# Performance work log

Hardware: AMD Instinct MI355X
Metric: run time of the kernel (lower is better)

Reference implementation:

```python
import jax, jax.numpy as jnp
import numpy as np

B, T, V, C, D = 32, 512, 25, 64, 128
EPS = 1e-5


def _shift_indices(num_nodes, ch, sign):
    i = np.arange(num_nodes)[:, None]
    j = np.arange(ch)[None, :]
    idx = (i * ch + j + sign * j * ch) % (ch * num_nodes)
    return jnp.asarray(idx.reshape(-1).astype(np.int32))


def setup_inputs() -> dict:
    key = jax.random.key(0)
    ks = jax.random.split(key, 6)
    return {
        "x0": jax.random.normal(ks[0], (B, T, V, C), jnp.float32),
        "feature_mask": jax.random.normal(ks[1], (1, V, C), jnp.float32) * 0.1,
        "W": jax.random.normal(ks[2], (C, D), jnp.float32) * (1.0 / np.sqrt(D)),
        "lin_b": jax.random.normal(ks[3], (1, 1, D), jnp.float32) * 0.02,
        "bn_gamma": jnp.ones((V * D,), jnp.float32),
        "bn_beta": jnp.zeros((V * D,), jnp.float32),
        "down_w": jax.random.normal(ks[4], (D, C), jnp.float32) * (1.0 / np.sqrt(C)),
        "down_b": jax.random.normal(ks[5], (D,), jnp.float32) * 0.02,
        "dbn_gamma": jnp.ones((D,), jnp.float32),
        "dbn_beta": jnp.zeros((D,), jnp.float32),
        "shift_in": _shift_indices(V, C, +1),
        "shift_out": _shift_indices(V, D, -1),
    }


def reference(x0, feature_mask, W, lin_b, bn_gamma, bn_beta,
              down_w, down_b, dbn_gamma, dbn_beta, shift_in, shift_out):
    b, t, v, c = x0.shape
    d = W.shape[1]
    n = b * t
    # shift-in gather over flattened (V*C) feature axis
    x = x0.reshape(n, v * c)[:, shift_in].reshape(n, v, c)
    # learned feature mask
    x = x * (jnp.tanh(feature_mask) + 1.0)
    # small per-node linear
    x = jnp.einsum('nvc,cd->nvd', x, W) + lin_b
    # shift-out gather
    x = x.reshape(n, v * d)[:, shift_out]
    # BatchNorm1d (training-mode batch stats, biased variance)
    mu = x.mean(0)
    var = x.var(0)
    x = (x - mu) * (bn_gamma / jnp.sqrt(var + EPS)) + bn_beta
    x = x.reshape(b, t, v, d).transpose(0, 3, 1, 2)  # (B, D, T, V)
    # residual down path: 1x1 conv == per-position matmul, then BN2d
    res = jnp.einsum('btvc,dc->btvd', x0, down_w) + down_b
    rmu = res.mean((0, 1, 2))
    rvar = res.var((0, 1, 2))
    res = (res - rmu) * (dbn_gamma / jnp.sqrt(rvar + EPS)) + dbn_beta
    res = res.transpose(0, 3, 1, 2)  # (B, D, T, V)
    return jax.nn.relu(x + res)
```

## Files before the change

kernel.cpp:

```cpp
#include <hip/hip_runtime.h>

#define VC 1600
#define EPSF 1e-5f

#define WS_MASKJ  0
#define WS_WPACK  1600
#define WS_DWPACK 5696
#define WS_ABY    9792
#define WS_ABR    16192
#define WS_COLSUM 16448
#define WS_QY     18048
#define WS_ABY2   1721984
#define WS_Y_SH   3456768
#define WS_R_SH   55885568
#define WS_NEED_BYTES 216628736ULL

typedef __attribute__((ext_vector_type(8))) short s16x8;
typedef __attribute__((ext_vector_type(4))) short s16x4;
typedef __attribute__((ext_vector_type(4))) float f32x4;

__device__ __forceinline__ short f2bf(float f) {
  unsigned u = __builtin_bit_cast(unsigned, f);
  u += 0x7fffu + ((u >> 16) & 1u);
  return (short)(u >> 16);
}
__device__ __forceinline__ float bf2f(short s) {
  unsigned u = ((unsigned)(unsigned short)s) << 16;
  return __builtin_bit_cast(float, u);
}

__device__ __forceinline__ void stage_elem(int j, int base, int vstr, float4 xv,
                                           const float* mj, short* s_raw, short* s_xm) {
  int u = j >> 6, c = j & 63;
  s16x4 pk; pk[0]=f2bf(xv.x); pk[1]=f2bf(xv.y); pk[2]=f2bf(xv.z); pk[3]=f2bf(xv.w);
  *(s16x4*)(s_raw + (base + u*vstr)*72 + c) = pk;
  int v0 = (u - c + 75) % 25;
  float xa[4] = {xv.x, xv.y, xv.z, xv.w};
#pragma unroll
  for (int e = 0; e < 4; e++) {
    int ve = v0 - e; if (ve < 0) ve += 25;
    s_xm[(base + ve*vstr)*72 + c + e] = f2bf(xa[e] * mj[e]);
  }
}

__global__ void k_init(const float* __restrict__ fm, const float* __restrict__ W,
                       const float* __restrict__ dw, float* __restrict__ ws) {
  int g = blockIdx.x * 256 + threadIdx.x;
  if (g < VC) {
    int c = g & 63, jv = g >> 6;
    int v = (jv - c + 75) % 25;
    ws[WS_MASKJ + g] = tanhf(fm[v * 64 + c]) + 1.0f;
    ws[WS_COLSUM + g] = 0.0f;
  }
  if (g < 3328) ws[WS_QY + g] = 0.0f;
  if (g >= 4096 && g < 5120) {
    int idx = g - 4096;
    int frag = idx >> 6, lane = idx & 63;
    int nt = frag >> 1, k = frag & 1, q = lane >> 4, l = lane & 15;
    s16x8 pk;
#pragma unroll
    for (int j = 0; j < 8; j++) {
      int c = k * 32 + q * 8 + j;
      pk[j] = f2bf(W[c * 128 + nt * 16 + l]);
    }
    ((s16x8*)(ws + WS_WPACK))[idx] = pk;
  }
  if (g >= 3328 && g < 4096) {
  }
  if (g >= 5120 - 1024 && g < 5120 && false) {}
  if (blockIdx.x >= 16) {
    int idx = (blockIdx.x - 16) * 256 + threadIdx.x;
    if (idx < 1024) {
      int frag = idx >> 6, lane = idx & 63;
      int nt = frag >> 1, k = frag & 1, q = lane >> 4, l = lane & 15;
      s16x8 pk;
#pragma unroll
      for (int j = 0; j < 8; j++) {
        int c = k * 32 + q * 8 + j;
        pk[j] = f2bf(dw[(nt * 16 + l) * 64 + c]);
      }
      ((s16x8*)(ws + WS_DWPACK))[idx] = pk;
    }
  }
}

__launch_bounds__(256, 2)
__global__ void k_stats(const float* __restrict__ x0, float* __restrict__ ws, int do_store) {
  __shared__ short s_raw[8064];
  __shared__ short s_xm[8064];
  int tid = threadIdx.x;
  int wave = tid >> 6, lane = tid & 63, quad = lane >> 4, l15 = lane & 15;
  for (int t = tid; t < 864; t += 256) { s_raw[7200 + t] = 0; s_xm[7200 + t] = 0; }
  const s16x8* wpack = (const s16x8*)(ws + WS_WPACK);
  const s16x8* dwpack = (const s16x8*)(ws + WS_DWPACK);
  short* wsy = (short*)ws + WS_Y_SH;
  short* wsr = (short*)ws + WS_R_SH;

  int nt0 = wave * 2;
  s16x8 bw[2][2], bd[2][2];
#pragma unroll
  for (int a = 0; a < 2; a++) {
    int nt = nt0 + a;
    bw[a][0] = wpack[(nt * 2 + 0) * 64 + lane];
    bw[a][1] = wpack[(nt * 2 + 1) * 64 + lane];
    bd[a][0] = dwpack[(nt * 2 + 0) * 64 + lane];
    bd[a][1] = dwpack[(nt * 2 + 1) * 64 + lane];
  }
  float mj0[4], mj1[4];
  {
    float4 m4 = *(const float4*)(ws + WS_MASKJ + tid * 4);
    mj0[0]=m4.x; mj0[1]=m4.y; mj0[2]=m4.z; mj0[3]=m4.w;
  }
  if (tid < 144) {
    float4 m4 = *(const float4*)(ws + WS_MASKJ + 1024 + tid * 4);
    mj1[0]=m4.x; mj1[1]=m4.y; mj1[2]=m4.z; mj1[3]=m4.w;
  }
  float cs[8] = {0,0,0,0,0,0,0,0};
  float rq0 = 0.f, rq1 = 0.f;
  float qy[7][2];
#pragma unroll
  for (int i = 0; i < 7; i++) { qy[i][0] = 0.f; qy[i][1] = 0.f; }

  for (int chunk = 0; chunk < 8; chunk++) {
    int n0 = blockIdx.x * 32 + chunk * 4;
    size_t cb = (size_t)(blockIdx.x * 8 + chunk) * 12800;
    __syncthreads();
    for (int r = 0; r < 4; r++) {
      const float* rowp = x0 + (size_t)(n0 + r) * VC;
      float4 xv = *(const float4*)(rowp + tid * 4);
      cs[0]+=xv.x; cs[1]+=xv.y; cs[2]+=xv.z; cs[3]+=xv.w;
      stage_elem(tid * 4, r, 4, xv, mj0, s_raw, s_xm);
      if (tid < 144) {
        float4 xw = *(const float4*)(rowp + 1024 + tid * 4);
        cs[4]+=xw.x; cs[5]+=xw.y; cs[6]+=xw.z; cs[7]+=xw.w;
        stage_elem(1024 + tid * 4, r, 4, xw, mj1, s_raw, s_xm);
      }
    }
    __syncthreads();
#pragma unroll
    for (int vp = 0; vp < 7; vp++) {
      int rb = vp * 16;
      const short* px = s_xm + (rb + l15) * 72 + quad * 8;
      const short* pr = s_raw + (rb + l15) * 72 + quad * 8;
      s16x8 a0 = *(const s16x8*)px;
      s16x8 a1 = *(const s16x8*)(px + 32);
      s16x8 r0 = *(const s16x8*)pr;
      s16x8 r1 = *(const s16x8*)(pr + 32);
#pragma unroll
      for (int a = 0; a < 2; a++) {
        f32x4 acc = {0.f, 0.f, 0.f, 0.f};
        acc = __builtin_amdgcn_mfma_f32_16x16x32_bf16(a0, bw[a][0], acc, 0, 0, 0);
        acc = __builtin_amdgcn_mfma_f32_16x16x32_bf16(a1, bw[a][1], acc, 0, 0, 0);
        qy[vp][a] += acc[0]*acc[0] + acc[1]*acc[1] + acc[2]*acc[2] + acc[3]*acc[3];
        f32x4 rc = {0.f, 0.f, 0.f, 0.f};
        rc = __builtin_amdgcn_mfma_f32_16x16x32_bf16(r0, bd[a][0], rc, 0, 0, 0);
        rc = __builtin_amdgcn_mfma_f32_16x16x32_bf16(r1, bd[a][1], rc, 0, 0, 0);
        float t2 = rc[0]*rc[0] + rc[1]*rc[1] + rc[2]*rc[2] + rc[3]*rc[3];
        if (a == 0) rq0 += t2; else rq1 += t2;
      }
      if (do_store) {
#pragma unroll
        for (int aa = 0; aa < 2; aa++) {
          f32x4 tY = {0.f, 0.f, 0.f, 0.f};
          tY = __builtin_amdgcn_mfma_f32_16x16x32_bf16(bw[aa][0], a0, tY, 0, 0, 0);
          tY = __builtin_amdgcn_mfma_f32_16x16x32_bf16(bw[aa][1], a1, tY, 0, 0, 0);
          f32x4 tR = {0.f, 0.f, 0.f, 0.f};
          tR = __builtin_amdgcn_mfma_f32_16x16x32_bf16(bd[aa][0], r0, tR, 0, 0, 0);
          tR = __builtin_amdgcn_mfma_f32_16x16x32_bf16(bd[aa][1], r1, tR, 0, 0, 0);
          s16x4 ky, kr;
#pragma unroll
          for (int e = 0; e < 4; e++) { ky[e] = f2bf(tY[e]); kr[e] = f2bf(tR[e]); }
          if (vp < 6) {
            int off = vp * 2048 + wave * 512 + aa * 256 + lane * 4;
            *(s16x4*)(wsy + cb + off) = ky;
            *(s16x4*)(wsr + cb + off) = kr;
          } else if (l15 < 4) {
            int off = 12288 + (wave * 2 + aa) * 64 + (quad * 4 + l15) * 4;
            *(s16x4*)(wsy + cb + off) = ky;
            *(s16x4*)(wsr + cb + off) = kr;
          }
        }
      }
    }
  }
  rq0 += __shfl_xor(rq0, 16); rq0 += __shfl_xor(rq0, 32);
  rq1 += __shfl_xor(rq1, 16); rq1 += __shfl_xor(rq1, 32);
  if (quad == 0) {
    atomicAdd(ws + WS_QY + 3200 + nt0 * 16 + l15, rq0);
    atomicAdd(ws + WS_QY + 3200 + (nt0 + 1) * 16 + l15, rq1);
  }
#pragma unroll
  for (int vp = 0; vp < 7; vp++) {
    int vq = vp * 4 + quad;
    if (vq < 25) {
      atomicAdd(ws + WS_QY + vq * 128 + nt0 * 16 + l15, qy[vp][0]);
      atomicAdd(ws + WS_QY + vq * 128 + (nt0 + 1) * 16 + l15, qy[vp][1]);
    }
  }
#pragma unroll
  for (int e = 0; e < 4; e++) atomicAdd(ws + WS_COLSUM + tid * 4 + e, cs[e]);
  if (tid < 144) {
#pragma unroll
    for (int e = 0; e < 4; e++) atomicAdd(ws + WS_COLSUM + 1024 + tid * 4 + e, cs[4 + e]);
  }
}

__global__ void k_reduce(const float* __restrict__ gamma, const float* __restrict__ beta,
                         const float* __restrict__ dgamma, const float* __restrict__ dbeta,
                         const float* __restrict__ W, const float* __restrict__ dw,
                         float* __restrict__ ws, int do_store) {
  int tid = threadIdx.x;
  if (blockIdx.x == 25) {
    __shared__ float s_cs[64];
    if (tid < 64) {
      float s = 0.f;
#pragma unroll
      for (int v = 0; v < 25; v++) s += ws[WS_COLSUM + v * 64 + tid];
      s_cs[tid] = s;
    }
    __syncthreads();
    if (tid >= 128) return;
    int d = tid;
    float q = ws[WS_QY + 3200 + d];
    float m = 0.f;
#pragma unroll 8
    for (int c = 0; c < 64; c++) m += s_cs[c] * dw[d * 64 + c];
    m *= (1.0f / 409600.0f);
    float var = q * (1.0f / 409600.0f) - m * m;
    float a = dgamma[d] * rsqrtf(var + EPSF);
    ((float2*)(ws + WS_ABR))[d] = make_float2(a, dbeta[d] - m * a);
    return;
  }
  __shared__ float s_cm[1600];
  for (int t = tid; t < 1600; t += 128)
    s_cm[t] = ws[WS_COLSUM + t] * ws[WS_MASKJ + t];
  __syncthreads();
  int f = blockIdx.x * 128 + tid;
  int v = f >> 7, d = f & 127;
  float q = ws[WS_QY + f];
  float m = 0.f;
  int p = v * 64;
#pragma unroll 8
  for (int c = 0; c < 64; c++) {
    m += s_cm[p] * W[c * 128 + d];
    p += 65; if (p >= VC) p -= VC;
  }
  m *= (1.0f / 16384.0f);
  float var = q * (1.0f / 16384.0f) - m * m;
  int d25 = d % 25;
  int vo = v + d25; if (vo >= 25) vo -= 25;
  int jg = vo * 128 + d;
  float a = gamma[jg] * rsqrtf(var + EPSF);
  float bb = beta[jg] - m * a;
  ((float2*)(ws + WS_ABY))[f] = make_float2(a, bb);
  if (do_store) ((float2*)(ws + WS_ABY2))[vo * 128 + d] = make_float2(a, bb);
}

__launch_bounds__(256, 3)
__global__ void k_out(const float* __restrict__ ws, float* __restrict__ out) {
  __shared__ short s_y[12800];
  __shared__ short s_r[12800];
  int tid = threadIdx.x;
  int bid = blockIdx.x;
  const short* wsy = (const short*)ws + WS_Y_SH + (size_t)bid * 12800;
  const short* wsr = (const short*)ws + WS_R_SH + (size_t)bid * 12800;
  for (int t = tid; t < 3200; t += 256) {
    int arr = (t >= 1600);
    int tt = arr ? (t - 1600) : t;
    const short* src = arr ? wsr : wsy;
    short* dst = arr ? s_r : s_y;
    s16x8 w = *(const s16x8*)(src + tt * 8);
#pragma unroll
    for (int h = 0; h < 2; h++) {
      int g = tt * 2 + h;
      int slot, d0;
      if (g < 3072) {
        int vp = g >> 9, rem = g & 511;
        int wv = rem >> 7, rem2 = rem & 127;
        int aa = rem2 >> 6, ln = rem2 & 63;
        slot = vp * 16 + (ln & 15);
        d0 = (wv * 2 + aa) * 16 + (ln >> 4) * 4;
      } else {
        int g2 = g - 3072;
        int cr = g2 >> 4, ci = g2 & 15;
        slot = 96 + (ci & 3);
        d0 = cr * 16 + (ci >> 2) * 4;
      }
      int v = slot >> 2, r = slot & 3;
      int L = r * 25 + v;
      int phys = ((L << 4) + ((d0 >> 3) ^ ((L * 5) & 15))) * 8 + (d0 & 7);
      s16x4 hh; hh[0] = w[h*4]; hh[1] = w[h*4+1]; hh[2] = w[h*4+2]; hh[3] = w[h*4+3];
      *(s16x4*)(dst + phys) = hh;
    }
  }
  __syncthreads();
  int n0 = bid * 4;
  int b = n0 >> 9, t0 = n0 & 511;
  float* ob = out + (size_t)b * 1638400 + (size_t)t0 * 25;
  const float2* aby2 = (const float2*)(ws + WS_ABY2);
  const float2* abrp = (const float2*)(ws + WS_ABR);
  for (int it = tid; it < 3200; it += 256) {
    int dd = it / 25;
    int qg = it - dd * 25;
    int q0 = qg * 4;
    int d25 = dd % 25;
    float2 ar = abrp[dd];
    int tl = q0 / 25;
    int vo = q0 - tl * 25;
    int sh = dd >> 3, dlo = dd & 7;
    float ov[4];
#pragma unroll
    for (int e = 0; e < 4; e++) {
      int vi = vo - d25; if (vi < 0) vi += 25;
      int Ly = tl * 25 + vi, Lr = tl * 25 + vo;
      int ady = ((Ly << 4) + (sh ^ ((Ly * 5) & 15))) * 8 + dlo;
      int adr = ((Lr << 4) + (sh ^ ((Lr * 5) & 15))) * 8 + dlo;
      float yv = bf2f(s_y[ady]);
      float rv = bf2f(s_r[adr]);
      float2 ay = aby2[vo * 128 + dd];
      ov[e] = fmaxf(yv * ay.x + ay.y + rv * ar.x + ar.y, 0.0f);
      vo++; if (vo == 25) { vo = 0; tl++; }
    }
    float4 o; o.x = ov[0]; o.y = ov[1]; o.z = ov[2]; o.w = ov[3];
    *(float4*)(ob + (size_t)dd * 12800 + q0) = o;
  }
}

__launch_bounds__(256, 2)
__global__ void k_main(const float* __restrict__ x0, const float* __restrict__ ws,
                       float* __restrict__ out) {
  __shared__ short s_raw[112 * 72];
  __shared__ short s_xm[112 * 72];
  __shared__ short s_ybuf[100 * 129];
  int tid = threadIdx.x;
  int wave = tid >> 6, lane = tid & 63, quad = lane >> 4, l15 = lane & 15;
  int n0 = blockIdx.x * 4;
  for (int t = tid; t < 1600; t += 256) {
    int flat = t * 4;
    int nl = flat / VC;
    int j = flat - nl * VC;
    float4 xv = *(const float4*)(x0 + (size_t)n0 * VC + flat);
    float4 m4 = *(const float4*)(ws + WS_MASKJ + j);
    float mj[4] = {m4.x, m4.y, m4.z, m4.w};
    stage_elem(j, nl * 25, 1, xv, mj, (short*)s_raw, (short*)s_xm);
  }
  __syncthreads();
  const s16x8* wpack = (const s16x8*)(ws + WS_WPACK);
  const float2* aby = (const float2*)(ws + WS_ABY);
  {
    s16x8 b0, b1;
#pragma unroll
    for (int ji = 0; ji < 14; ji++) {
      int job = wave * 14 + ji;
      int nt = job / 7, mt = job - nt * 7;
      if (ji == 0 || ji == 7) {
        b0 = wpack[(nt * 2 + 0) * 64 + lane];
        b1 = wpack[(nt * 2 + 1) * 64 + lane];
      }
      int mbase = mt * 16;
      const short* pa = s_xm + (mbase + l15) * 72 + quad * 8;
      s16x8 a0 = *(const s16x8*)(pa);
      s16x8 a1 = *(const s16x8*)(pa + 32);
      f32x4 acc = {0.f, 0.f, 0.f, 0.f};
      acc = __builtin_amdgcn_mfma_f32_16x16x32_bf16(a0, b0, acc, 0, 0, 0);
      acc = __builtin_amdgcn_mfma_f32_16x16x32_bf16(a1, b1, acc, 0, 0, 0);
      int d = nt * 16 + l15;
      int d25 = d % 25;
#pragma unroll
      for (int i = 0; i < 4; i++) {
        int s = mbase + quad * 4 + i;
        if (s < 100) {
          int r = s / 25;
          int vv = s - r * 25;
          float2 ab = aby[vv * 128 + d];
          float val = acc[i] * ab.x + ab.y;
          int vo = vv + d25; if (vo >= 25) vo -= 25;
          s_ybuf[(r * 25 + vo) * 129 + d] = f2bf(val);
        }
      }
    }
  }
  __syncthreads();
  const s16x8* dwpack = (const s16x8*)(ws + WS_DWPACK);
  const float2* abr = (const float2*)(ws + WS_ABR);
  {
    s16x8 b0, b1; float2 ab = make_float2(0.f, 0.f);
#pragma unroll
    for (int ji = 0; ji < 14; ji++) {
      int job = wave * 14 + ji;
      int nt = job / 7, mt = job - nt * 7;
      if (ji == 0 || ji == 7) {
        b0 = dwpack[(nt * 2 + 0) * 64 + lane];
        b1 = dwpack[(nt * 2 + 1) * 64 + lane];
        ab = abr[nt * 16 + l15];
      }
      int mbase = mt * 16;
      const short* pa = s_raw + (mbase + l15) * 72 + quad * 8;
      s16x8 a0 = *(const s16x8*)(pa);
      s16x8 a1 = *(const s16x8*)(pa + 32);
      f32x4 acc = {0.f, 0.f, 0.f, 0.f};
      acc = __builtin_amdgcn_mfma_f32_16x16x32_bf16(a0, b0, acc, 0, 0, 0);
      acc = __builtin_amdgcn_mfma_f32_16x16x32_bf16(a1, b1, acc, 0, 0, 0);
      int d = nt * 16 + l15;
#pragma unroll
      for (int i = 0; i < 4; i++) {
        int s = mbase + quad * 4 + i;
        if (s < 100) {
          int r = s / 25;
          int vv = s - r * 25;
          int ad = (r * 25 + vv) * 129 + d;
          float val = acc[i] * ab.x + ab.y + bf2f(s_ybuf[ad]);
          val = fmaxf(val, 0.0f);
          s_ybuf[ad] = f2bf(val);
        }
      }
    }
  }
  __syncthreads();
  int b = n0 >> 9, t0 = n0 & 511;
  float* ob = out + (size_t)b * 1638400 + (size_t)t0 * 25;
  for (int it = tid; it < 3200; it += 256) {
    int dd = it / 25;
    int qg = it - dd * 25;
    int q0 = qg * 4;
    float4 o;
    o.x = bf2f(s_ybuf[(q0 + 0) * 129 + dd]);
    o.y = bf2f(s_ybuf[(q0 + 1) * 129 + dd]);
    o.z = bf2f(s_ybuf[(q0 + 2) * 129 + dd]);
    o.w = bf2f(s_ybuf[(q0 + 3) * 129 + dd]);
    *(float4*)(ob + (size_t)dd * 12800 + q0) = o;
  }
}

extern "C" void kernel_launch(void* const* d_in, const int* in_sizes, int n_in,
                              void* d_out, int out_size, void* d_ws, size_t ws_size,
                              hipStream_t stream) {
  const float* x0    = (const float*)d_in[0];
  const float* fm    = (const float*)d_in[1];
  const float* W     = (const float*)d_in[2];
  const float* bn_g  = (const float*)d_in[4];
  const float* bn_b  = (const float*)d_in[5];
  const float* dw    = (const float*)d_in[6];
  const float* dbn_g = (const float*)d_in[8];
  const float* dbn_b = (const float*)d_in[9];
  float* ws = (float*)d_ws;
  float* out = (float*)d_out;
  int big = (ws_size >= WS_NEED_BYTES) ? 1 : 0;
  k_init<<<20, 256, 0, stream>>>(fm, W, dw, ws);
  k_stats<<<512, 256, 0, stream>>>(x0, ws, big);
  k_reduce<<<26, 128, 0, stream>>>(bn_g, bn_b, dbn_g, dbn_b, W, dw, ws, big);
  if (big) k_out<<<4096, 256, 0, stream>>>(ws, out);
  else     k_main<<<4096, 256, 0, stream>>>(x0, ws, out);
}
```

Measured before the change: 564.7 us.

## Store interleaved y/res intermediates in output order and simplify output pass

k_stats now transposes the bf16 y and residual tiles through shared memory into an interleaved, output-ordered (d, t, v) layout with the shift-out permutation already applied, then writes them contiguously. k_out becomes a streaming pass that reads one vector, applies a precomputed per-position float4 of combined scale and bias coefficients, and writes output without a shared-memory shuffle. The reduce kernel is split so the big path fuses both BN coefficient sets into one table. This moves permutation work into the stats kernel and adds extra shared-memory scatter and syncs there. The scatter uses scalar 2-byte stores that may bank-conflict.

```diff
diff --git a/kernel.cpp b/kernel.cpp
--- a/kernel.cpp
+++ b/kernel.cpp
@@ -10,9 +10,8 @@
 #define WS_ABR    16192
 #define WS_COLSUM 16448
 #define WS_QY     18048
-#define WS_ABY2   1721984
-#define WS_Y_SH   3456768
-#define WS_R_SH   55885568
+#define WS_CFL    24576
+#define WS_YR_SH  153600
 #define WS_NEED_BYTES 216628736ULL
 
 typedef __attribute__((ext_vector_type(8))) short s16x8;
@@ -53,8 +52,8 @@
     ws[WS_COLSUM + g] = 0.0f;
   }
   if (g < 3328) ws[WS_QY + g] = 0.0f;
-  if (g >= 4096 && g < 5120) {
-    int idx = g - 4096;
+  if (g >= 3328 && g < 4352) {
+    int idx = g - 3328;
     int frag = idx >> 6, lane = idx & 63;
     int nt = frag >> 1, k = frag & 1, q = lane >> 4, l = lane & 15;
     s16x8 pk;
@@ -65,36 +64,29 @@
     }
     ((s16x8*)(ws + WS_WPACK))[idx] = pk;
   }
-  if (g >= 3328 && g < 4096) {
-  }
-  if (g >= 5120 - 1024 && g < 5120 && false) {}
-  if (blockIdx.x >= 16) {
-    int idx = (blockIdx.x - 16) * 256 + threadIdx.x;
-    if (idx < 1024) {
-      int frag = idx >> 6, lane = idx & 63;
-      int nt = frag >> 1, k = frag & 1, q = lane >> 4, l = lane & 15;
-      s16x8 pk;
-#pragma unroll
-      for (int j = 0; j < 8; j++) {
-        int c = k * 32 + q * 8 + j;
-        pk[j] = f2bf(dw[(nt * 16 + l) * 64 + c]);
-      }
-      ((s16x8*)(ws + WS_DWPACK))[idx] = pk;
-    }
+  if (g >= 4352 && g < 5376) {
+    int idx = g - 4352;
+    int frag = idx >> 6, lane = idx & 63;
+    int nt = frag >> 1, k = frag & 1, q = lane >> 4, l = lane & 15;
+    s16x8 pk;
+#pragma unroll
+    for (int j = 0; j < 8; j++) {
+      int c = k * 32 + q * 8 + j;
+      pk[j] = f2bf(dw[(nt * 16 + l) * 64 + c]);
+    }
+    ((s16x8*)(ws + WS_DWPACK))[idx] = pk;
   }
 }
 
 __launch_bounds__(256, 2)
 __global__ void k_stats(const float* __restrict__ x0, float* __restrict__ ws, int do_store) {
-  __shared__ short s_raw[8064];
-  __shared__ short s_xm[8064];
+  __shared__ __align__(16) short s_mem[25600];
+  short* s_raw = s_mem;
+  short* s_xm  = s_mem + 8064;
   int tid = threadIdx.x;
   int wave = tid >> 6, lane = tid & 63, quad = lane >> 4, l15 = lane & 15;
-  for (int t = tid; t < 864; t += 256) { s_raw[7200 + t] = 0; s_xm[7200 + t] = 0; }
   const s16x8* wpack = (const s16x8*)(ws + WS_WPACK);
   const s16x8* dwpack = (const s16x8*)(ws + WS_DWPACK);
-  short* wsy = (short*)ws + WS_Y_SH;
-  short* wsr = (short*)ws + WS_R_SH;
 
   int nt0 = wave * 2;
   s16x8 bw[2][2], bd[2][2];
@@ -120,10 +112,11 @@
   float qy[7][2];
 #pragma unroll
   for (int i = 0; i < 7; i++) { qy[i][0] = 0.f; qy[i][1] = 0.f; }
+  s16x4 kyv[7][2], krv[7][2];
 
   for (int chunk = 0; chunk < 8; chunk++) {
     int n0 = blockIdx.x * 32 + chunk * 4;
-    size_t cb = (size_t)(blockIdx.x * 8 + chunk) * 12800;
+    int cg = blockIdx.x * 8 + chunk;
     __syncthreads();
     for (int r = 0; r < 4; r++) {
       const float* rowp = x0 + (size_t)(n0 + r) * VC;
@@ -156,7 +149,7 @@
         rc = __builtin_amdgcn_mfma_f32_16x16x32_bf16(r0, bd[a][0], rc, 0, 0, 0);
         rc = __builtin_amdgcn_mfma_f32_16x16x32_bf16(r1, bd[a][1], rc, 0, 0, 0);
         float t2 = rc[0]*rc[0] + rc[1]*rc[1] + rc[2]*rc[2] + rc[3]*rc[3];
-        if (a == 0) rq0 += t2; else rq1 += t2;
+        if (vp < 6 || quad == 0) { if (a == 0) rq0 += t2; else rq1 += t2; }
       }
       if (do_store) {
 #pragma unroll
@@ -170,17 +163,39 @@
           s16x4 ky, kr;
 #pragma unroll
           for (int e = 0; e < 4; e++) { ky[e] = f2bf(tY[e]); kr[e] = f2bf(tR[e]); }
-          if (vp < 6) {
-            int off = vp * 2048 + wave * 512 + aa * 256 + lane * 4;
-            *(s16x4*)(wsy + cb + off) = ky;
-            *(s16x4*)(wsr + cb + off) = kr;
-          } else if (l15 < 4) {
-            int off = 12288 + (wave * 2 + aa) * 64 + (quad * 4 + l15) * 4;
-            *(s16x4*)(wsy + cb + off) = ky;
-            *(s16x4*)(wsr + cb + off) = kr;
+          kyv[vp][aa] = ky; krv[vp][aa] = kr;
+        }
+      }
+    }
+    __syncthreads();
+    if (do_store) {
+#pragma unroll
+      for (int vp = 0; vp < 7; vp++) {
+        if (vp < 6 || l15 < 4) {
+          int slot = vp * 16 + l15;
+          int v = slot >> 2, r = slot & 3;
+          int Lr = r * 25 + v;
+#pragma unroll
+          for (int aa = 0; aa < 2; aa++) {
+            int d0 = (nt0 + aa) * 16 + quad * 4;
+            int d25 = d0 % 25;
+#pragma unroll
+            for (int e = 0; e < 4; e++) {
+              int d = d0 + e;
+              int de = d25 + e; if (de >= 25) de -= 25;
+              int vo = v + de; if (vo >= 25) vo -= 25;
+              s_mem[(d * 100 + r * 25 + vo) * 2]     = kyv[vp][aa][e];
+              s_mem[(d * 100 + Lr) * 2 + 1]          = krv[vp][aa][e];
+            }
           }
         }
       }
+    }
+    __syncthreads();
+    if (do_store) {
+      short* gyr = (short*)ws + WS_YR_SH + (size_t)cg * 25600;
+      for (int t = tid; t < 3200; t += 256)
+        *(s16x8*)(gyr + t * 8) = *(const s16x8*)(s_mem + t * 8);
     }
   }
   rq0 += __shfl_xor(rq0, 16); rq0 += __shfl_xor(rq0, 32);
@@ -205,10 +220,52 @@
   }
 }
 
-__global__ void k_reduce(const float* __restrict__ gamma, const float* __restrict__ beta,
-                         const float* __restrict__ dgamma, const float* __restrict__ dbeta,
-                         const float* __restrict__ W, const float* __restrict__ dw,
-                         float* __restrict__ ws, int do_store) {
+__global__ void k_reduce_big(const float* __restrict__ gamma, const float* __restrict__ beta,
+                             const float* __restrict__ dgamma, const float* __restrict__ dbeta,
+                             const float* __restrict__ W, const float* __restrict__ dw,
+                             float* __restrict__ ws) {
+  __shared__ float s_cm[1600];
+  __shared__ float s_cs[64];
+  int tid = threadIdx.x;
+  for (int t = tid; t < 1600; t += 128) s_cm[t] = ws[WS_COLSUM + t] * ws[WS_MASKJ + t];
+  if (tid < 64) {
+    float s = 0.f;
+#pragma unroll
+    for (int v2 = 0; v2 < 25; v2++) s += ws[WS_COLSUM + v2 * 64 + tid];
+    s_cs[tid] = s;
+  }
+  __syncthreads();
+  int v = blockIdx.x, d = tid;
+  float q = ws[WS_QY + v * 128 + d];
+  float m = 0.f;
+  int p = v * 64;
+#pragma unroll 8
+  for (int c = 0; c < 64; c++) { m += s_cm[p] * W[c * 128 + d]; p += 65; if (p >= VC) p -= VC; }
+  m *= (1.0f / 16384.0f);
+  float var = q * (1.0f / 16384.0f) - m * m;
+  int d25 = d % 25;
+  int vo = v + d25; if (vo >= 25) vo -= 25;
+  int jg = vo * 128 + d;
+  float ay = gamma[jg] * rsqrtf(var + EPSF);
+  float by = beta[jg] - m * ay;
+  float qr = ws[WS_QY + 3200 + d];
+  float mr = 0.f;
+#pragma unroll 8
+  for (int c = 0; c < 64; c++) mr += s_cs[c] * dw[d * 64 + c];
+  mr *= (1.0f / 409600.0f);
+  float varr = qr * (1.0f / 409600.0f) - mr * mr;
+  float ar = dgamma[d] * rsqrtf(varr + EPSF);
+  float br = dbeta[d] - mr * ar;
+  float4 c4 = make_float4(ay, by + br, ar, 0.f);
+#pragma unroll
+  for (int r = 0; r < 4; r++)
+    ((float4*)(ws + WS_CFL))[d * 100 + r * 25 + vo] = c4;
+}
+
+__global__ void k_reduce_f(const float* __restrict__ gamma, const float* __restrict__ beta,
+                           const float* __restrict__ dgamma, const float* __restrict__ dbeta,
+                           const float* __restrict__ W, const float* __restrict__ dw,
+                           float* __restrict__ ws) {
   int tid = threadIdx.x;
   if (blockIdx.x == 25) {
     __shared__ float s_cs[64];
@@ -251,78 +308,28 @@
   int vo = v + d25; if (vo >= 25) vo -= 25;
   int jg = vo * 128 + d;
   float a = gamma[jg] * rsqrtf(var + EPSF);
-  float bb = beta[jg] - m * a;
-  ((float2*)(ws + WS_ABY))[f] = make_float2(a, bb);
-  if (do_store) ((float2*)(ws + WS_ABY2))[vo * 128 + d] = make_float2(a, bb);
-}
-
-__launch_bounds__(256, 3)
+  ((float2*)(ws + WS_ABY))[f] = make_float2(a, beta[jg] - m * a);
+}
+
 __global__ void k_out(const float* __restrict__ ws, float* __restrict__ out) {
-  __shared__ short s_y[12800];
-  __shared__ short s_r[12800];
-  int tid = threadIdx.x;
-  int bid = blockIdx.x;
-  const short* wsy = (const short*)ws + WS_Y_SH + (size_t)bid * 12800;
-  const short* wsr = (const short*)ws + WS_R_SH + (size_t)bid * 12800;
-  for (int t = tid; t < 3200; t += 256) {
-    int arr = (t >= 1600);
-    int tt = arr ? (t - 1600) : t;
-    const short* src = arr ? wsr : wsy;
-    short* dst = arr ? s_r : s_y;
-    s16x8 w = *(const s16x8*)(src + tt * 8);
-#pragma unroll
-    for (int h = 0; h < 2; h++) {
-      int g = tt * 2 + h;
-      int slot, d0;
-      if (g < 3072) {
-        int vp = g >> 9, rem = g & 511;
-        int wv = rem >> 7, rem2 = rem & 127;
-        int aa = rem2 >> 6, ln = rem2 & 63;
-        slot = vp * 16 + (ln & 15);
-        d0 = (wv * 2 + aa) * 16 + (ln >> 4) * 4;
-      } else {
-        int g2 = g - 3072;
-        int cr = g2 >> 4, ci = g2 & 15;
-        slot = 96 + (ci & 3);
-        d0 = cr * 16 + (ci >> 2) * 4;
-      }
-      int v = slot >> 2, r = slot & 3;
-      int L = r * 25 + v;
-      int phys = ((L << 4) + ((d0 >> 3) ^ ((L * 5) & 15))) * 8 + (d0 & 7);
-      s16x4 hh; hh[0] = w[h*4]; hh[1] = w[h*4+1]; hh[2] = w[h*4+2]; hh[3] = w[h*4+3];
-      *(s16x4*)(dst + phys) = hh;
-    }
-  }
-  __syncthreads();
-  int n0 = bid * 4;
+  int tid = threadIdx.x, cg = blockIdx.x;
+  const short* gyr = (const short*)ws + WS_YR_SH + (size_t)cg * 25600;
+  const float4* cfl = (const float4*)(ws + WS_CFL);
+  int n0 = cg * 4;
   int b = n0 >> 9, t0 = n0 & 511;
   float* ob = out + (size_t)b * 1638400 + (size_t)t0 * 25;
-  const float2* aby2 = (const float2*)(ws + WS_ABY2);
-  const float2* abrp = (const float2*)(ws + WS_ABR);
-  for (int it = tid; it < 3200; it += 256) {
-    int dd = it / 25;
-    int qg = it - dd * 25;
-    int q0 = qg * 4;
-    int d25 = dd % 25;
-    float2 ar = abrp[dd];
-    int tl = q0 / 25;
-    int vo = q0 - tl * 25;
-    int sh = dd >> 3, dlo = dd & 7;
+  for (int t = tid; t < 3200; t += 256) {
+    s16x8 w = *(const s16x8*)(gyr + t * 8);
     float ov[4];
 #pragma unroll
-    for (int e = 0; e < 4; e++) {
-      int vi = vo - d25; if (vi < 0) vi += 25;
-      int Ly = tl * 25 + vi, Lr = tl * 25 + vo;
-      int ady = ((Ly << 4) + (sh ^ ((Ly * 5) & 15))) * 8 + dlo;
-      int adr = ((Lr << 4) + (sh ^ ((Lr * 5) & 15))) * 8 + dlo;
-      float yv = bf2f(s_y[ady]);
-      float rv = bf2f(s_r[adr]);
-      float2 ay = aby2[vo * 128 + dd];
-      ov[e] = fmaxf(yv * ay.x + ay.y + rv * ar.x + ar.y, 0.0f);
-      vo++; if (vo == 25) { vo = 0; tl++; }
-    }
+    for (int j = 0; j < 4; j++) {
+      float4 c4 = cfl[t * 4 + j];
+      ov[j] = fmaxf(bf2f(w[2 * j]) * c4.x + bf2f(w[2 * j + 1]) * c4.z + c4.y, 0.0f);
+    }
+    int d = t / 25;
+    int L0 = (t - d * 25) * 4;
     float4 o; o.x = ov[0]; o.y = ov[1]; o.z = ov[2]; o.w = ov[3];
-    *(float4*)(ob + (size_t)dd * 12800 + q0) = o;
+    *(float4*)(ob + (size_t)d * 12800 + L0) = o;
   }
 }
 
@@ -446,9 +453,13 @@
   float* ws = (float*)d_ws;
   float* out = (float*)d_out;
   int big = (ws_size >= WS_NEED_BYTES) ? 1 : 0;
-  k_init<<<20, 256, 0, stream>>>(fm, W, dw, ws);
+  k_init<<<21, 256, 0, stream>>>(fm, W, dw, ws);
   k_stats<<<512, 256, 0, stream>>>(x0, ws, big);
-  k_reduce<<<26, 128, 0, stream>>>(bn_g, bn_b, dbn_g, dbn_b, W, dw, ws, big);
-  if (big) k_out<<<4096, 256, 0, stream>>>(ws, out);
-  else     k_main<<<4096, 256, 0, stream>>>(x0, ws, out);
-}
+  if (big) {
+    k_reduce_big<<<25, 128, 0, stream>>>(bn_g, bn_b, dbn_g, dbn_b, W, dw, ws);
+    k_out<<<4096, 256, 0, stream>>>(ws, out);
+  } else {
+    k_reduce_f<<<26, 128, 0, stream>>>(bn_g, bn_b, dbn_g, dbn_b, W, dw, ws);
+    k_main<<<4096, 256, 0, stream>>>(x0, ws, out);
+  }
+}
```

Result: slower. 786.2 us (+39.2%).
